# Kernel tuning notes

Hardware: AMD Instinct MI355X
Metric: run time of the kernel (lower is better)

## Reference

```python
import jax, jax.numpy as jnp
import numpy as np

B, D0, D1, D2 = 512, 4096, 4096, 4096
W_SCALE = 0.01  # small init so sigmoids stay in a useful range


def setup_inputs() -> dict:
    key = jax.random.key(0)
    k0, k1, k2, k3, k4 = jax.random.split(key, 5)
    return {
        "data": jax.random.uniform(k0, (B, D0), dtype=jnp.float32),
        "W1": jax.random.normal(k1, (D0, D1), dtype=jnp.float32) * W_SCALE,
        "W2": jax.random.normal(k2, (D1, D2), dtype=jnp.float32) * W_SCALE,
        "b1": jax.random.normal(k3, (D1,), dtype=jnp.float32),
        "b2": jax.random.normal(k4, (D2,), dtype=jnp.float32),
        "iterations": 10,
    }


def reference(data, W1, W2, b1, b2, iterations):
    """Mean-field conditional sample of a 3-layer DBM (visible clamped to data).

    Faithful to conditional_sample_general_meanfield with mean_cond (sigmoid
    of bias + interaction), sample_state[0]=False, invtemperature=1.0.
    Schedule per iteration: odd layers (j=1) then even layers (j=2).
    """
    beta = jnp.float32(1.0)
    nb = data.shape[0]
    # initial states: layer mean activations broadcast over the batch
    s1 = jnp.broadcast_to(jax.nn.sigmoid(b1), (nb, b1.shape[0]))
    s2 = jnp.broadcast_to(jax.nn.sigmoid(b2), (nb, b2.shape[0]))

    def gibbs_step(carry, _):
        s1, s2 = carry
        # j=1: interaction from below (gradOutput: data @ W1) and above (gradInput: s2 @ W2^T)
        s1 = jax.nn.sigmoid(b1 + beta * (data @ W1 + s2 @ W2.T))
        # j=2: interaction from below (gradOutput: s1 @ W2); j=0 clamped
        s2 = jax.nn.sigmoid(b2 + beta * (s1 @ W2))
        return (s1, s2), None

    (s1, s2), _ = jax.lax.scan(gibbs_step, (s1, s2), None, length=iterations)
    # original returns [state0, state1, state2]; state0 == data (clamped)
    return jnp.stack([s1, s2])  # [2, B, D]
```

## Files before the change

### kernel.cpp

```cpp
#include <hip/hip_runtime.h>


typedef __bf16 bf16_t;
typedef __attribute__((ext_vector_type(8))) __bf16 bf16x8;
typedef __attribute__((ext_vector_type(4))) float f32x4;
typedef __attribute__((ext_vector_type(2))) _Float16 half2v;

typedef const __attribute__((address_space(1))) void* gptr_t;
typedef __attribute__((address_space(3))) void* lptr_t;

constexpr int M = 512, N = 4096, K = 4096;
constexpr int BM = 128, BN = 128, BK = 32;
constexpr int SPLIT = 8;
constexpr int PHASES = K / (SPLIT * BK);
constexpr int NTILES = (M / BM) * (N / BN);
constexpr int TILE_H2 = BM * BN / 2;


__global__ __launch_bounds__(256) void prep_w(const float* __restrict__ in,
                                              bf16_t* __restrict__ outT,
                                              bf16_t* __restrict__ outC) {
  __shared__ float t[64][65];
  const int tid = threadIdx.x;
  const int x0 = blockIdx.x * 64, y0 = blockIdx.y * 64;
  const int row = tid >> 4;
  const int xs  = tid & 15;
#pragma unroll
  for (int i = 0; i < 4; ++i) {
    const int r = row + 16 * i;
    float4 v = *(const float4*)(in + (size_t)(y0 + r) * 4096 + x0 + xs * 4);
    t[xs * 4 + 0][r] = v.x;
    t[xs * 4 + 1][r] = v.y;
    t[xs * 4 + 2][r] = v.z;
    t[xs * 4 + 3][r] = v.w;
  }
  __syncthreads();
#pragma unroll
  for (int j = 0; j < 2; ++j) {
    const int idx = tid + 256 * j;
    const int xr = idx >> 3, sg = idx & 7;
    bf16x8 v;
#pragma unroll
    for (int e = 0; e < 8; ++e) v[e] = (bf16_t)t[xr][sg * 8 + e];
    *(bf16x8*)(outT + (size_t)(x0 + xr) * 4096 + y0 + sg * 8) = v;
  }
  if (outC) {
#pragma unroll
    for (int j = 0; j < 2; ++j) {
      const int idx = tid + 256 * j;
      const int yr = idx >> 3, sg = idx & 7;
      bf16x8 v;
#pragma unroll
      for (int e = 0; e < 8; ++e) v[e] = (bf16_t)t[sg * 8 + e][yr];
      *(bf16x8*)(outC + (size_t)(y0 + yr) * 4096 + x0 + sg * 8) = v;
    }
  }
}

__global__ __launch_bounds__(256) void cvt_bf16(const float* __restrict__ in,
                                                bf16_t* __restrict__ out) {
  const size_t i8 = ((size_t)blockIdx.x * 256 + threadIdx.x) * 8;
  float4 a = *(const float4*)(in + i8);
  float4 b = *(const float4*)(in + i8 + 4);
  bf16x8 o;
  o[0] = (bf16_t)a.x; o[1] = (bf16_t)a.y; o[2] = (bf16_t)a.z; o[3] = (bf16_t)a.w;
  o[4] = (bf16_t)b.x; o[5] = (bf16_t)b.y; o[6] = (bf16_t)b.z; o[7] = (bf16_t)b.w;
  *(bf16x8*)(out + i8) = o;
}

__global__ __launch_bounds__(256) void init_s2(const float* __restrict__ b2,
                                               bf16_t* __restrict__ s2, int total) {
  int i = blockIdx.x * 256 + threadIdx.x;
  if (i < total) {
    float x = b2[i & (N - 1)];
    s2[i] = (bf16_t)(1.0f / (1.0f + __expf(-x)));
  }
}

__global__ __launch_bounds__(256, 4) void gemm_bt(
    const bf16_t* __restrict__ A,
    const bf16_t* __restrict__ BT,
    _Float16* __restrict__ slabs) {
  __shared__ __align__(16) bf16_t sA[2 * BM * BK];
  __shared__ __align__(16) bf16_t sB[2 * BN * BK];

  const int gid = blockIdx.x;
  const int g = gid >> 5, rr5 = gid & 31;
  const int y = rr5 >> 3, c = rr5 & 7;
  const int txz = g * 8 + c;
  const int x = txz & 31, z = txz >> 5;
  const int tile = y * 32 + x;

  const int tid = threadIdx.x;
  const int wid = tid >> 6;
  const int l   = tid & 63;
  const int r   = l & 15;
  const int q   = l >> 4;
  const int wm  = wid & 1;
  const int wn  = wid >> 1;

  const int m0 = y * BM;
  const int n0 = x * BN;

  const bf16_t* Ab = A + (size_t)m0 * K + (size_t)z * (PHASES * BK);
  const bf16_t* Bb = BT + (size_t)n0 * K + (size_t)z * (PHASES * BK);

  const int srow = l >> 2;
  const int scol = (l & 3) * 8;

  f32x4 acc[4][4];
  const f32x4 zero = {0.0f, 0.0f, 0.0f, 0.0f};
#pragma unroll
  for (int i = 0; i < 4; ++i)
#pragma unroll
    for (int j = 0; j < 4; ++j) acc[i][j] = zero;

  auto issue = [&](int ph, int pb) {
    const size_t kof = (size_t)ph * BK;
#pragma unroll
    for (int cc = 0; cc < 2; ++cc) {
      const int ch = wid + cc * 4;
      __builtin_amdgcn_global_load_lds(
          (gptr_t)(Ab + (size_t)(ch * 16 + srow) * K + kof + scol),
          (lptr_t)(sA + pb * 4096 + ch * 512), 16, 0, 0);
      __builtin_amdgcn_global_load_lds(
          (gptr_t)(Bb + (size_t)(ch * 16 + srow) * K + kof + scol),
          (lptr_t)(sB + pb * 4096 + ch * 512), 16, 0, 0);
    }
  };

  issue(0, 0);
  for (int ph = 0; ph < PHASES; ++ph) {
    const int pb = ph & 1;
    __syncthreads();
    if (ph + 1 < PHASES) issue(ph + 1, pb ^ 1);

    bf16x8 af[4], bfr[4];
#pragma unroll
    for (int mt = 0; mt < 4; ++mt)
      af[mt] = *(const bf16x8*)(sA + pb * 4096 + (wm * 64 + mt * 16 + r) * BK + q * 8);
#pragma unroll
    for (int nt = 0; nt < 4; ++nt)
      bfr[nt] = *(const bf16x8*)(sB + pb * 4096 + (wn * 64 + nt * 16 + r) * BK + q * 8);

#pragma unroll
    for (int mt = 0; mt < 4; ++mt)
#pragma unroll
      for (int nt = 0; nt < 4; ++nt)
        acc[mt][nt] = __builtin_amdgcn_mfma_f32_16x16x32_bf16(
            af[mt], bfr[nt], acc[mt][nt], 0, 0, 0);
  }

  half2v* P2 = (half2v*)slabs + ((size_t)z * NTILES + tile) * TILE_H2;
#pragma unroll
  for (int mt = 0; mt < 4; ++mt)
#pragma unroll
    for (int nt = 0; nt < 4; ++nt)
#pragma unroll
      for (int i2 = 0; i2 < 2; ++i2) {
        half2v h;
        h[0] = (_Float16)acc[mt][nt][2 * i2];
        h[1] = (_Float16)acc[mt][nt][2 * i2 + 1];
        P2[(((wid * 4 + mt) * 4 + nt) * 2 + i2) * 64 + l] = h;
      }
}

template <int MODE>
__global__ __launch_bounds__(256) void epi(const _Float16* __restrict__ slabs,
                                           const float* __restrict__ bias,
                                           const bf16_t* __restrict__ C0b,
                                           bf16_t* __restrict__ outb,
                                           float* __restrict__ outf) {
  const int t = blockIdx.x * 256 + threadIdx.x;
  const int tile = t >> 13;
  const int s = t & 8191;
  float v0 = 0.0f, v1 = 0.0f;
#pragma unroll
  for (int z = 0; z < SPLIT; ++z) {
    half2v h = ((const half2v*)slabs)[((size_t)z * NTILES + tile) * TILE_H2 + s];
    v0 += (float)h[0];
    v1 += (float)h[1];
  }
  const int l = s & 63, i2 = (s >> 6) & 1, nt = (s >> 7) & 3, mt = (s >> 9) & 3,
            wid = s >> 11;
  const int q = l >> 4, r = l & 15, wm = wid & 1, wn = wid >> 1;
  const int row = (tile >> 5) * 128 + wm * 64 + mt * 16 + q * 4 + 2 * i2;
  const int col = (tile & 31) * 128 + wn * 64 + nt * 16 + r;
  const size_t i0 = (size_t)row * N + col;
  const size_t i1 = i0 + N;
  if (MODE == 0) {
    outb[i0] = (bf16_t)v0;
    outb[i1] = (bf16_t)v1;
    return;
  }
  const float bv = bias[col];
  v0 += bv; v1 += bv;
  if (MODE == 1) {
    v0 += (float)C0b[i0];
    v1 += (float)C0b[i1];
  }
  const float s0 = 1.0f / (1.0f + __expf(-v0));
  const float s1 = 1.0f / (1.0f + __expf(-v1));
  outb[i0] = (bf16_t)s0;
  outb[i1] = (bf16_t)s1;
  if (outf) {
    outf[i0] = s0;
    outf[i1] = s1;
  }
}


extern "C" void kernel_launch(void* const* d_in, const int* in_sizes, int n_in,
                              void* d_out, int out_size, void* d_ws, size_t ws_size,
                              hipStream_t stream) {
  const float* data = (const float*)d_in[0];
  const float* W1   = (const float*)d_in[1];
  const float* W2   = (const float*)d_in[2];
  const float* b1   = (const float*)d_in[3];
  const float* b2   = (const float*)d_in[4];

  char* p = (char*)d_ws;
  bf16_t* W1T = (bf16_t*)p; p += (size_t)K * N * 2;
  bf16_t* W2b = (bf16_t*)p; p += (size_t)K * N * 2;
  bf16_t* W2T = (bf16_t*)p; p += (size_t)K * N * 2;
  bf16_t* C0b = (bf16_t*)p; p += (size_t)M * N * 2;
  bf16_t* s1b = (bf16_t*)p; p += (size_t)M * N * 2;
  bf16_t* s2b = (bf16_t*)p; p += (size_t)M * N * 2;
  bf16_t* dat = (bf16_t*)p; p += (size_t)M * K * 2;

  _Float16* slabC = (_Float16*)W2T;
  _Float16* slab  = (_Float16*)W1T;

  float* out_s1 = (float*)d_out;
  float* out_s2 = out_s1 + (size_t)M * N;

  cvt_bf16<<<(M * K) / 2048, 256, 0, stream>>>(data, dat);
  prep_w<<<dim3(64, 64), 256, 0, stream>>>(W1, W1T, (bf16_t*)nullptr);

  const int gblocks = 32 * 4 * SPLIT;
  const int epiblocks = (M * N / 2) / 256;

  gemm_bt<<<gblocks, 256, 0, stream>>>(dat, W1T, slabC);
  epi<0><<<epiblocks, 256, 0, stream>>>(slabC, nullptr, nullptr, C0b, nullptr);

  prep_w<<<dim3(64, 64), 256, 0, stream>>>(W2, W2T, W2b);
  init_s2<<<(M * N) / 256, 256, 0, stream>>>(b2, s2b, M * N);

  for (int it = 0; it < 10; ++it) {
    const bool last = (it == 9);
    gemm_bt<<<gblocks, 256, 0, stream>>>(s2b, W2b, slab);
    epi<1><<<epiblocks, 256, 0, stream>>>(slab, b1, C0b, s1b,
                                          last ? out_s1 : (float*)nullptr);
    gemm_bt<<<gblocks, 256, 0, stream>>>(s1b, W2T, slab);
    epi<2><<<epiblocks, 256, 0, stream>>>(slab, b2, nullptr, s2b,
                                          last ? out_s2 : (float*)nullptr);
  }
}
```

Baseline: 898.1 us.

## Enlarge GEMM tiles to 256x256x64 with swizzled LDS and vectorized epilogue

The split-K GEMM grows from 128x128x32 tiles with 256 threads to 256x256x64 tiles with 512 threads (8 waves, each holding 8x4 MFMA accumulators). This raises data reuse per LDS load and cuts global traffic per FLOP. LDS rows are XOR-swizzled to avoid bank conflicts, and partial-sum slabs are written with nontemporal stores. The reduction epilogue now handles four columns per thread with vector loads and stores. The catch is a grid of only 256 blocks using 128KB of LDS each, so there is roughly one block per CU and less latency hiding.

New measurement: 802.6 us. 10.6% less time.

```diff
diff --git a/kernel.cpp b/kernel.cpp
--- a/kernel.cpp
+++ b/kernel.cpp
@@ -3,16 +3,19 @@
 
 typedef __bf16 bf16_t;
 typedef __attribute__((ext_vector_type(8))) __bf16 bf16x8;
+typedef __attribute__((ext_vector_type(4))) __bf16 bf16x4;
 typedef __attribute__((ext_vector_type(4))) float f32x4;
 typedef __attribute__((ext_vector_type(2))) _Float16 half2v;
+typedef __attribute__((ext_vector_type(8))) _Float16 f16x8;
 
 typedef const __attribute__((address_space(1))) void* gptr_t;
 typedef __attribute__((address_space(3))) void* lptr_t;
 
 constexpr int M = 512, N = 4096, K = 4096;
-constexpr int BM = 128, BN = 128, BK = 32;
+constexpr int BM = 256, BN = 256, BK = 64;
 constexpr int SPLIT = 8;
-constexpr int PHASES = K / (SPLIT * BK);
+constexpr int KSLICE = K / SPLIT;
+constexpr int PHASES = KSLICE / BK;
 constexpr int NTILES = (M / BM) * (N / BN);
 constexpr int TILE_H2 = BM * BN / 2;
 
@@ -77,7 +80,7 @@
   }
 }
 
-__global__ __launch_bounds__(256, 4) void gemm_bt(
+__global__ __launch_bounds__(512, 2) void gemm_bt(
     const bf16_t* __restrict__ A,
     const bf16_t* __restrict__ BT,
     _Float16* __restrict__ slabs) {
@@ -85,11 +88,11 @@
   __shared__ __align__(16) bf16_t sB[2 * BN * BK];
 
   const int gid = blockIdx.x;
-  const int g = gid >> 5, rr5 = gid & 31;
-  const int y = rr5 >> 3, c = rr5 & 7;
-  const int txz = g * 8 + c;
-  const int x = txz & 31, z = txz >> 5;
-  const int tile = y * 32 + x;
+  const int z = gid & 7;
+  const int rem = gid >> 3;
+  const int tx = rem & 15;
+  const int ty = rem >> 4;
+  const int tile = ty * 16 + tx;
 
   const int tid = threadIdx.x;
   const int wid = tid >> 6;
@@ -99,33 +102,31 @@
   const int wm  = wid & 1;
   const int wn  = wid >> 1;
 
-  const int m0 = y * BM;
-  const int n0 = x * BN;
-
-  const bf16_t* Ab = A + (size_t)m0 * K + (size_t)z * (PHASES * BK);
-  const bf16_t* Bb = BT + (size_t)n0 * K + (size_t)z * (PHASES * BK);
-
-  const int srow = l >> 2;
-  const int scol = (l & 3) * 8;
-
-  f32x4 acc[4][4];
+  const bf16_t* Ab = A + (size_t)(ty * BM) * K + (size_t)z * KSLICE;
+  const bf16_t* Bb = BT + (size_t)(tx * BN) * K + (size_t)z * KSLICE;
+
+  const int srow8 = l >> 3;
+  const int scol  = ((l & 7) ^ srow8) * 8;
+
+  f32x4 acc[8][4];
   const f32x4 zero = {0.0f, 0.0f, 0.0f, 0.0f};
 #pragma unroll
-  for (int i = 0; i < 4; ++i)
+  for (int i = 0; i < 8; ++i)
 #pragma unroll
     for (int j = 0; j < 4; ++j) acc[i][j] = zero;
 
   auto issue = [&](int ph, int pb) {
     const size_t kof = (size_t)ph * BK;
 #pragma unroll
-    for (int cc = 0; cc < 2; ++cc) {
-      const int ch = wid + cc * 4;
+    for (int i = 0; i < 4; ++i) {
+      const int rg = wid * 4 + i;
+      const int row = rg * 8 + srow8;
       __builtin_amdgcn_global_load_lds(
-          (gptr_t)(Ab + (size_t)(ch * 16 + srow) * K + kof + scol),
-          (lptr_t)(sA + pb * 4096 + ch * 512), 16, 0, 0);
+          (gptr_t)(Ab + (size_t)row * K + kof + scol),
+          (lptr_t)(sA + pb * (BM * BK) + rg * 512), 16, 0, 0);
       __builtin_amdgcn_global_load_lds(
-          (gptr_t)(Bb + (size_t)(ch * 16 + srow) * K + kof + scol),
-          (lptr_t)(sB + pb * 4096 + ch * 512), 16, 0, 0);
+          (gptr_t)(Bb + (size_t)row * K + kof + scol),
+          (lptr_t)(sB + pb * (BN * BK) + rg * 512), 16, 0, 0);
     }
   };
 
@@ -135,25 +136,35 @@
     __syncthreads();
     if (ph + 1 < PHASES) issue(ph + 1, pb ^ 1);
 
-    bf16x8 af[4], bfr[4];
-#pragma unroll
-    for (int mt = 0; mt < 4; ++mt)
-      af[mt] = *(const bf16x8*)(sA + pb * 4096 + (wm * 64 + mt * 16 + r) * BK + q * 8);
-#pragma unroll
-    for (int nt = 0; nt < 4; ++nt)
-      bfr[nt] = *(const bf16x8*)(sB + pb * 4096 + (wn * 64 + nt * 16 + r) * BK + q * 8);
-
-#pragma unroll
-    for (int mt = 0; mt < 4; ++mt)
-#pragma unroll
-      for (int nt = 0; nt < 4; ++nt)
-        acc[mt][nt] = __builtin_amdgcn_mfma_f32_16x16x32_bf16(
-            af[mt], bfr[nt], acc[mt][nt], 0, 0, 0);
+    const bf16_t* sAp = sA + pb * (BM * BK);
+    const bf16_t* sBp = sB + pb * (BN * BK);
+#pragma unroll
+    for (int kk = 0; kk < 2; ++kk) {
+      bf16x8 af[8], bfr[4];
+#pragma unroll
+      for (int mt = 0; mt < 8; ++mt) {
+        const int rowm = wm * 128 + mt * 16 + r;
+        const int sl = (kk * 4 + q) ^ (r & 7);
+        af[mt] = *(const bf16x8*)(sAp + rowm * BK + sl * 8);
+      }
+#pragma unroll
+      for (int nt = 0; nt < 4; ++nt) {
+        const int rown = wn * 64 + nt * 16 + r;
+        const int sl = (kk * 4 + q) ^ (r & 7);
+        bfr[nt] = *(const bf16x8*)(sBp + rown * BK + sl * 8);
+      }
+#pragma unroll
+      for (int mt = 0; mt < 8; ++mt)
+#pragma unroll
+        for (int nt = 0; nt < 4; ++nt)
+          acc[mt][nt] = __builtin_amdgcn_mfma_f32_16x16x32_bf16(
+              af[mt], bfr[nt], acc[mt][nt], 0, 0, 0);
+    }
   }
 
   half2v* P2 = (half2v*)slabs + ((size_t)z * NTILES + tile) * TILE_H2;
 #pragma unroll
-  for (int mt = 0; mt < 4; ++mt)
+  for (int mt = 0; mt < 8; ++mt)
 #pragma unroll
     for (int nt = 0; nt < 4; ++nt)
 #pragma unroll
@@ -161,7 +172,8 @@
         half2v h;
         h[0] = (_Float16)acc[mt][nt][2 * i2];
         h[1] = (_Float16)acc[mt][nt][2 * i2 + 1];
-        P2[(((wid * 4 + mt) * 4 + nt) * 2 + i2) * 64 + l] = h;
+        __builtin_nontemporal_store(
+            h, P2 + (size_t)((((wid * 8 + mt) * 4 + nt) * 2 + i2) * 64 + l));
       }
 }
 
@@ -171,41 +183,69 @@
                                            const bf16_t* __restrict__ C0b,
                                            bf16_t* __restrict__ outb,
                                            float* __restrict__ outf) {
-  const int t = blockIdx.x * 256 + threadIdx.x;
-  const int tile = t >> 13;
-  const int s = t & 8191;
-  float v0 = 0.0f, v1 = 0.0f;
-#pragma unroll
-  for (int z = 0; z < SPLIT; ++z) {
-    half2v h = ((const half2v*)slabs)[((size_t)z * NTILES + tile) * TILE_H2 + s];
-    v0 += (float)h[0];
-    v1 += (float)h[1];
-  }
-  const int l = s & 63, i2 = (s >> 6) & 1, nt = (s >> 7) & 3, mt = (s >> 9) & 3,
-            wid = s >> 11;
-  const int q = l >> 4, r = l & 15, wm = wid & 1, wn = wid >> 1;
-  const int row = (tile >> 5) * 128 + wm * 64 + mt * 16 + q * 4 + 2 * i2;
-  const int col = (tile & 31) * 128 + wn * 64 + nt * 16 + r;
+  const int g = blockIdx.x * 256 + threadIdx.x;
+  const int tile = g >> 13;
+  const int gi = g & 8191;
+  const int slot = gi >> 4;
+  const int l4 = (gi & 15) * 4;
+
+  float s0[4] = {0.f, 0.f, 0.f, 0.f};
+  float s1[4] = {0.f, 0.f, 0.f, 0.f};
+  const size_t ubase = (size_t)tile * TILE_H2 + slot * 64 + l4;
+#pragma unroll
+  for (int zz = 0; zz < SPLIT; ++zz) {
+    f16x8 v = *(const f16x8*)((const half2v*)slabs +
+                              (size_t)zz * NTILES * TILE_H2 + ubase);
+#pragma unroll
+    for (int j = 0; j < 4; ++j) {
+      s0[j] += (float)v[2 * j];
+      s1[j] += (float)v[2 * j + 1];
+    }
+  }
+
+  const int i2 = slot & 1, nt = (slot >> 1) & 3, mt = (slot >> 3) & 7,
+            wid = slot >> 6;
+  const int wm = wid & 1, wn = wid >> 1;
+  const int q = (gi & 15) >> 2, rb = (gi & 3) * 4;
+  const int ty = tile >> 4, tx = tile & 15;
+  const int row = ty * 256 + wm * 128 + mt * 16 + q * 4 + 2 * i2;
+  const int col = tx * 256 + wn * 64 + nt * 16 + rb;
   const size_t i0 = (size_t)row * N + col;
   const size_t i1 = i0 + N;
+
   if (MODE == 0) {
-    outb[i0] = (bf16_t)v0;
-    outb[i1] = (bf16_t)v1;
+    bf16x4 o0, o1;
+#pragma unroll
+    for (int j = 0; j < 4; ++j) { o0[j] = (bf16_t)s0[j]; o1[j] = (bf16_t)s1[j]; }
+    *(bf16x4*)(outb + i0) = o0;
+    *(bf16x4*)(outb + i1) = o1;
     return;
   }
-  const float bv = bias[col];
-  v0 += bv; v1 += bv;
+  const float4 bv = *(const float4*)(bias + col);
+  s0[0] += bv.x; s0[1] += bv.y; s0[2] += bv.z; s0[3] += bv.w;
+  s1[0] += bv.x; s1[1] += bv.y; s1[2] += bv.z; s1[3] += bv.w;
   if (MODE == 1) {
-    v0 += (float)C0b[i0];
-    v1 += (float)C0b[i1];
-  }
-  const float s0 = 1.0f / (1.0f + __expf(-v0));
-  const float s1 = 1.0f / (1.0f + __expf(-v1));
-  outb[i0] = (bf16_t)s0;
-  outb[i1] = (bf16_t)s1;
+    bf16x4 c0 = *(const bf16x4*)(C0b + i0);
+    bf16x4 c1 = *(const bf16x4*)(C0b + i1);
+#pragma unroll
+    for (int j = 0; j < 4; ++j) { s0[j] += (float)c0[j]; s1[j] += (float)c1[j]; }
+  }
+  float v0[4], v1[4];
+  bf16x4 o0, o1;
+#pragma unroll
+  for (int j = 0; j < 4; ++j) {
+    v0[j] = 1.0f / (1.0f + __expf(-s0[j]));
+    v1[j] = 1.0f / (1.0f + __expf(-s1[j]));
+    o0[j] = (bf16_t)v0[j];
+    o1[j] = (bf16_t)v1[j];
+  }
+  *(bf16x4*)(outb + i0) = o0;
+  *(bf16x4*)(outb + i1) = o1;
   if (outf) {
-    outf[i0] = s0;
-    outf[i1] = s1;
+    float4 f0 = {v0[0], v0[1], v0[2], v0[3]};
+    float4 f1 = {v1[0], v1[1], v1[2], v1[3]};
+    *(float4*)(outf + i0) = f0;
+    *(float4*)(outf + i1) = f1;
   }
 }
 
@@ -237,10 +277,10 @@
   cvt_bf16<<<(M * K) / 2048, 256, 0, stream>>>(data, dat);
   prep_w<<<dim3(64, 64), 256, 0, stream>>>(W1, W1T, (bf16_t*)nullptr);
 
-  const int gblocks = 32 * 4 * SPLIT;
-  const int epiblocks = (M * N / 2) / 256;
-
-  gemm_bt<<<gblocks, 256, 0, stream>>>(dat, W1T, slabC);
+  const int gblocks = NTILES * SPLIT;
+  const int epiblocks = (M * N / 8) / 256;
+
+  gemm_bt<<<gblocks, 512, 0, stream>>>(dat, W1T, slabC);
   epi<0><<<epiblocks, 256, 0, stream>>>(slabC, nullptr, nullptr, C0b, nullptr);
 
   prep_w<<<dim3(64, 64), 256, 0, stream>>>(W2, W2T, W2b);
@@ -248,10 +288,10 @@
 
   for (int it = 0; it < 10; ++it) {
     const bool last = (it == 9);
-    gemm_bt<<<gblocks, 256, 0, stream>>>(s2b, W2b, slab);
+    gemm_bt<<<gblocks, 512, 0, stream>>>(s2b, W2b, slab);
     epi<1><<<epiblocks, 256, 0, stream>>>(slab, b1, C0b, s1b,
                                           last ? out_s1 : (float*)nullptr);
-    gemm_bt<<<gblocks, 256, 0, stream>>>(s1b, W2T, slab);
+    gemm_bt<<<gblocks, 512, 0, stream>>>(s1b, W2T, slab);
     epi<2><<<epiblocks, 256, 0, stream>>>(slab, b2, nullptr, s2b,
                                           last ? out_s2 : (float*)nullptr);
   }
```
